# Performance work log

Hardware: AMD Instinct MI355X
Metric: run time of the kernel (lower is better)

The kernel has to match this reference:

```python
import jax, jax.numpy as jnp
import numpy as np

CUBIC_A = -0.75  # torch bicubic kernel coefficient


def _cubic(d):
    a = CUBIC_A
    ad = jnp.abs(d)
    near = (a + 2.0) * ad**3 - (a + 3.0) * ad**2 + 1.0
    far = a * (ad**3 - 5.0 * ad**2 + 8.0 * ad - 4.0)
    return jnp.where(ad <= 1.0, near, jnp.where(ad < 2.0, far, 0.0))


def _axis_weights(in_size, out_size):
    # half-pixel centers (align_corners=False), 4-tap cubic, edge clamp (matches torch)
    scale = in_size / out_size
    src = (jnp.arange(out_size, dtype=jnp.float32) + 0.5) * scale - 0.5
    i0 = jnp.floor(src).astype(jnp.int32)
    offs = jnp.arange(-1, 3)
    taps = i0[:, None] + offs[None, :]          # (out, 4)
    idx = jnp.clip(taps, 0, in_size - 1)
    w = _cubic(src[:, None] - taps.astype(jnp.float32))
    return idx, w


def _bicubic(img, h, w):
    # img: (H, W, C) -> (h, w, C), separable bicubic
    H, W, _ = img.shape
    ih, wh = _axis_weights(H, h)
    iw, ww = _axis_weights(W, w)
    rows = jnp.einsum('ot,otwc->owc', wh, img[ih])   # (h, W, C)
    out = jnp.einsum('ot,hotc->hoc', ww, rows[:, iw])  # (h, w, C)
    return out


def _sincos_1d(embed_dim, t_size):
    omega = np.arange(embed_dim // 2, dtype=np.float32) / (embed_dim / 2.0)
    omega = 1.0 / 10000 ** omega
    out = np.einsum('m,d->md', np.arange(t_size, dtype=np.float32), omega)
    return np.concatenate([np.sin(out), np.cos(out)], axis=1)


HEIGHT, WIDTH, NUM_FRAMES, DIM = 64, 64, 16, 1024
GRIDS = [(8, 32, 32), (8, 48, 48), (4, 64, 64), (1, 64, 64)]


def setup_inputs() -> dict:
    key = jax.random.key(0)
    k1, k2 = jax.random.split(key)
    total = sum(t * h * w for t, h, w in GRIDS)  # 47104
    x = jax.random.normal(k1, (total, DIM), dtype=jnp.float32)
    weight = jax.random.normal(k2, (HEIGHT, WIDTH, DIM), dtype=jnp.float32) * 0.02
    time_weight = jnp.asarray(_sincos_1d(DIM, NUM_FRAMES))[:, None, :]  # (T, 1, dim)
    grid_thws = jnp.asarray(GRIDS, dtype=jnp.int64)
    return {"x": x, "weight": weight, "time_weight": time_weight, "grid_thws": grid_thws}


def reference(x, weight, time_weight, grid_thws):
    H, W, dim = weight.shape
    grids = np.asarray(grid_thws).tolist()  # static per-sample shapes
    pos_embs = []
    for t, h, w in grids:
        if (h, w) == (H, W):
            pe2 = weight.reshape(-1, dim)
        else:
            pe2 = _bicubic(weight, h, w).reshape(-1, dim)
        if t == 1:
            pe3 = pe2
        else:
            pe3 = pe2[None, :, :] + time_weight[:t]  # (t, h*w, dim)
        pos_embs.append(pe3.reshape(-1, dim))
    return x + jnp.concatenate(pos_embs, axis=0)
```

## Files before the change

### kernel.cpp

```cpp
#include <hip/hip_runtime.h>

#define CUBIC_A (-0.75f)

__device__ __forceinline__ float cubic_w(float d) {
    float ad = fabsf(d);
    if (ad <= 1.0f) return ((CUBIC_A + 2.0f) * ad - (CUBIC_A + 3.0f)) * ad * ad + 1.0f;
    if (ad < 2.0f)  return CUBIC_A * (((ad - 5.0f) * ad + 8.0f) * ad - 4.0f);
    return 0.0f;
}

__global__ __launch_bounds__(256) void posemb_add_kernel(
    const float4* __restrict__ x,
    const float4* __restrict__ wgt,
    const float4* __restrict__ tw,
    float4* __restrict__ out)
{
    const int b  = blockIdx.x;
    const int d4 = threadIdx.x;

    int t, out_hw, px;
    long rowbase;
    int ppf;
    bool interp;
    if (b < 1024)      { t = 8; out_hw = 32; px = b;        rowbase = 0;     ppf = 1024; interp = true;  }
    else if (b < 3328) { t = 8; out_hw = 48; px = b - 1024; rowbase = 8192;  ppf = 2304; interp = true;  }
    else if (b < 7424) { t = 4; out_hw = 64; px = b - 3328; rowbase = 26624; ppf = 4096; interp = false; }
    else               { t = 1; out_hw = 64; px = b - 7424; rowbase = 43008; ppf = 4096; interp = false; }

    float4 pe;
    if (!interp) {
        pe = wgt[(size_t)px * 256 + d4];
    } else {
        const int i = px / out_hw;
        const int j = px % out_hw;
        const float scale = 64.0f / (float)out_hw;
        const float si = ((float)i + 0.5f) * scale - 0.5f;
        const float sj = ((float)j + 0.5f) * scale - 0.5f;
        const int i0 = (int)floorf(si);
        const int j0 = (int)floorf(sj);
        int ih[4], iw[4];
        float wh[4], ww[4];
#pragma unroll
        for (int a = 0; a < 4; ++a) {
            int tp = i0 - 1 + a;
            wh[a] = cubic_w(si - (float)tp);
            ih[a] = min(63, max(0, tp));
            tp = j0 - 1 + a;
            ww[a] = cubic_w(sj - (float)tp);
            iw[a] = min(63, max(0, tp));
        }
        float ax = 0.f, ay = 0.f, az = 0.f, aw = 0.f;
#pragma unroll
        for (int a = 0; a < 4; ++a) {
            float rx = 0.f, ry = 0.f, rz = 0.f, rw = 0.f;
#pragma unroll
            for (int c = 0; c < 4; ++c) {
                const float4 v = wgt[(size_t)(ih[a] * 64 + iw[c]) * 256 + d4];
                rx = fmaf(ww[c], v.x, rx);
                ry = fmaf(ww[c], v.y, ry);
                rz = fmaf(ww[c], v.z, rz);
                rw = fmaf(ww[c], v.w, rw);
            }
            ax = fmaf(wh[a], rx, ax);
            ay = fmaf(wh[a], ry, ay);
            az = fmaf(wh[a], rz, az);
            aw = fmaf(wh[a], rw, aw);
        }
        pe = make_float4(ax, ay, az, aw);
    }

    if (t > 1) {
        for (int f = 0; f < t; ++f) {
            const size_t row = (size_t)rowbase + (size_t)f * ppf + px;
            const float4 xv = x[row * 256 + d4];
            const float4 tv = tw[(size_t)f * 256 + d4];
            out[row * 256 + d4] = make_float4(xv.x + pe.x + tv.x,
                                              xv.y + pe.y + tv.y,
                                              xv.z + pe.z + tv.z,
                                              xv.w + pe.w + tv.w);
        }
    } else {
        const size_t row = (size_t)rowbase + px;
        const float4 xv = x[row * 256 + d4];
        out[row * 256 + d4] = make_float4(xv.x + pe.x,
                                          xv.y + pe.y,
                                          xv.z + pe.z,
                                          xv.w + pe.w);
    }
}

extern "C" void kernel_launch(void* const* d_in, const int* in_sizes, int n_in,
                              void* d_out, int out_size, void* d_ws, size_t ws_size,
                              hipStream_t stream) {
    const float4* x   = (const float4*)d_in[0];
    const float4* wgt = (const float4*)d_in[1];
    const float4* tw  = (const float4*)d_in[2];
    float4* out = (float4*)d_out;
    posemb_add_kernel<<<11520, 256, 0, stream>>>(x, wgt, tw, out);
}
```

Measured before the change: 89.32 us.

## Launch one block per output row and use nontemporal stores

```diff
diff --git a/kernel.cpp b/kernel.cpp
--- a/kernel.cpp
+++ b/kernel.cpp
@@ -1,6 +1,14 @@
 #include <hip/hip_runtime.h>
 
 #define CUBIC_A (-0.75f)
+
+typedef float f4nt __attribute__((ext_vector_type(4)));
+
+__device__ __forceinline__ void nt_store4(float4* p, float4 v) {
+    f4nt t;
+    t.x = v.x; t.y = v.y; t.z = v.z; t.w = v.w;
+    __builtin_nontemporal_store(t, (f4nt*)p);
+}
 
 __device__ __forceinline__ float cubic_w(float d) {
     float ad = fabsf(d);
@@ -9,84 +17,88 @@
     return 0.0f;
 }
 
+__device__ __forceinline__ float4 bicubic_pe(const float4* __restrict__ wgt,
+                                             int px, int out_hw, int d4) {
+    const int i = px / out_hw;
+    const int j = px % out_hw;
+    const float scale = 64.0f / (float)out_hw;
+    const float si = ((float)i + 0.5f) * scale - 0.5f;
+    const float sj = ((float)j + 0.5f) * scale - 0.5f;
+    const int i0 = (int)floorf(si);
+    const int j0 = (int)floorf(sj);
+    int ih[4], iw[4];
+    float wh[4], ww[4];
+#pragma unroll
+    for (int a = 0; a < 4; ++a) {
+        int tp = i0 - 1 + a;
+        wh[a] = cubic_w(si - (float)tp);
+        ih[a] = min(63, max(0, tp));
+        tp = j0 - 1 + a;
+        ww[a] = cubic_w(sj - (float)tp);
+        iw[a] = min(63, max(0, tp));
+    }
+    float ax = 0.f, ay = 0.f, az = 0.f, aw = 0.f;
+#pragma unroll
+    for (int a = 0; a < 4; ++a) {
+        float rx = 0.f, ry = 0.f, rz = 0.f, rw = 0.f;
+#pragma unroll
+        for (int c = 0; c < 4; ++c) {
+            const float4 v = wgt[(size_t)(ih[a] * 64 + iw[c]) * 256 + d4];
+            rx = fmaf(ww[c], v.x, rx);
+            ry = fmaf(ww[c], v.y, ry);
+            rz = fmaf(ww[c], v.z, rz);
+            rw = fmaf(ww[c], v.w, rw);
+        }
+        ax = fmaf(wh[a], rx, ax);
+        ay = fmaf(wh[a], ry, ay);
+        az = fmaf(wh[a], rz, az);
+        aw = fmaf(wh[a], rw, aw);
+    }
+    return make_float4(ax, ay, az, aw);
+}
+
 __global__ __launch_bounds__(256) void posemb_add_kernel(
     const float4* __restrict__ x,
     const float4* __restrict__ wgt,
     const float4* __restrict__ tw,
     float4* __restrict__ out)
 {
-    const int b  = blockIdx.x;
-    const int d4 = threadIdx.x;
+    const int row = blockIdx.x;
+    const int d4  = threadIdx.x;
 
-    int t, out_hw, px;
-    long rowbase;
-    int ppf;
-    bool interp;
-    if (b < 1024)      { t = 8; out_hw = 32; px = b;        rowbase = 0;     ppf = 1024; interp = true;  }
-    else if (b < 3328) { t = 8; out_hw = 48; px = b - 1024; rowbase = 8192;  ppf = 2304; interp = true;  }
-    else if (b < 7424) { t = 4; out_hw = 64; px = b - 3328; rowbase = 26624; ppf = 4096; interp = false; }
-    else               { t = 1; out_hw = 64; px = b - 7424; rowbase = 43008; ppf = 4096; interp = false; }
+    const size_t e = (size_t)row * 256 + d4;
+    const float4 xv = x[e];
 
     float4 pe;
-    if (!interp) {
+    float4 tv = make_float4(0.f, 0.f, 0.f, 0.f);
+
+    if (row < 8192) {
+        const int f  = row >> 10;
+        const int px = row & 1023;
+        tv = tw[(size_t)f * 256 + d4];
+        pe = bicubic_pe(wgt, px, 32, d4);
+    } else if (row < 26624) {
+        const int r  = row - 8192;
+        const int f  = r / 2304;
+        const int px = r - f * 2304;
+        tv = tw[(size_t)f * 256 + d4];
+        pe = bicubic_pe(wgt, px, 48, d4);
+    } else if (row < 43008) {
+        const int r  = row - 26624;
+        const int f  = r >> 12;
+        const int px = r & 4095;
+        tv = tw[(size_t)f * 256 + d4];
         pe = wgt[(size_t)px * 256 + d4];
     } else {
-        const int i = px / out_hw;
-        const int j = px % out_hw;
-        const float scale = 64.0f / (float)out_hw;
-        const float si = ((float)i + 0.5f) * scale - 0.5f;
-        const float sj = ((float)j + 0.5f) * scale - 0.5f;
-        const int i0 = (int)floorf(si);
-        const int j0 = (int)floorf(sj);
-        int ih[4], iw[4];
-        float wh[4], ww[4];
-#pragma unroll
-        for (int a = 0; a < 4; ++a) {
-            int tp = i0 - 1 + a;
-            wh[a] = cubic_w(si - (float)tp);
-            ih[a] = min(63, max(0, tp));
-            tp = j0 - 1 + a;
-            ww[a] = cubic_w(sj - (float)tp);
-            iw[a] = min(63, max(0, tp));
-        }
-        float ax = 0.f, ay = 0.f, az = 0.f, aw = 0.f;
-#pragma unroll
-        for (int a = 0; a < 4; ++a) {
-            float rx = 0.f, ry = 0.f, rz = 0.f, rw = 0.f;
-#pragma unroll
-            for (int c = 0; c < 4; ++c) {
-                const float4 v = wgt[(size_t)(ih[a] * 64 + iw[c]) * 256 + d4];
-                rx = fmaf(ww[c], v.x, rx);
-                ry = fmaf(ww[c], v.y, ry);
-                rz = fmaf(ww[c], v.z, rz);
-                rw = fmaf(ww[c], v.w, rw);
-            }
-            ax = fmaf(wh[a], rx, ax);
-            ay = fmaf(wh[a], ry, ay);
-            az = fmaf(wh[a], rz, az);
-            aw = fmaf(wh[a], rw, aw);
-        }
-        pe = make_float4(ax, ay, az, aw);
+        const int px = row - 43008;
+        pe = wgt[(size_t)px * 256 + d4];
     }
 
-    if (t > 1) {
-        for (int f = 0; f < t; ++f) {
-            const size_t row = (size_t)rowbase + (size_t)f * ppf + px;
-            const float4 xv = x[row * 256 + d4];
-            const float4 tv = tw[(size_t)f * 256 + d4];
-            out[row * 256 + d4] = make_float4(xv.x + pe.x + tv.x,
-                                              xv.y + pe.y + tv.y,
-                                              xv.z + pe.z + tv.z,
-                                              xv.w + pe.w + tv.w);
-        }
-    } else {
-        const size_t row = (size_t)rowbase + px;
-        const float4 xv = x[row * 256 + d4];
-        out[row * 256 + d4] = make_float4(xv.x + pe.x,
-                                          xv.y + pe.y,
-                                          xv.z + pe.z,
-                                          xv.w + pe.w);
-    }
+    nt_store4(&((float4*)out)[e],
+              make_float4(xv.x + pe.x + tv.x,
+                          xv.y + pe.y + tv.y,
+                          xv.z + pe.z + tv.z,
+                          xv.w + pe.w + tv.w));
 }
 
 extern "C" void kernel_launch(void* const* d_in, const int* in_sizes, int n_in,
@@ -96,5 +108,5 @@
     const float4* wgt = (const float4*)d_in[1];
     const float4* tw  = (const float4*)d_in[2];
     float4* out = (float4*)d_out;
-    posemb_add_kernel<<<11520, 256, 0, stream>>>(x, wgt, tw, out);
+    posemb_add_kernel<<<47104, 256, 0, stream>>>(x, wgt, tw, out);
 }
```

Result: slower. 141.4 us (+58.3%).
